# Kernel tuning notes

Measured on AMD Instinct MI355X. Metric: run time of the kernel, lower is better.

Reference implementation:

```python
import jax, jax.numpy as jnp
import numpy as np

B, S, D, P = 4, 2048, 1024, 1024

def setup_inputs() -> dict:
    key = jax.random.key(0)
    k1, k2, k3, k4 = jax.random.split(key, 4)
    x = jax.random.normal(k1, (B, S, D), dtype=jnp.float32)
    # nn.Linear weight is (out, in); store transposed (in, out) for x @ W
    scale = 1.0 / np.sqrt(D)
    Wq = jax.random.normal(k2, (D, P), dtype=jnp.float32) * scale
    Wk = jax.random.normal(k3, (D, P), dtype=jnp.float32) * scale
    Wv = jax.random.normal(k4, (D, P), dtype=jnp.float32) * scale
    return {"x": x, "Wq": Wq, "Wk": Wk, "Wv": Wv}

def reference(x, Wq, Wk, Wv):
    # projections (no bias)
    q = x @ Wq  # (B,S,P)
    k = x @ Wk
    v = x @ Wv
    scores = jnp.einsum('bsd,btd->bst', q, k)  # (B,S,S)
    seq = x.shape[1]
    causal = jnp.triu(jnp.ones((seq, seq), dtype=bool), k=1)
    scores = jnp.where(causal, -jnp.inf, scores)
    scores = scores / jnp.sqrt(jnp.asarray(P, dtype=scores.dtype))
    attn = jax.nn.softmax(scores, axis=-1)
    # dropout_prob=0.0 -> identity
    context = jnp.einsum('bst,btd->bsd', attn, v)  # (B,S,P)
    return context
```

## Files before the change

kernel.cpp:

```cpp
#include <hip/hip_runtime.h>
#include <hip/hip_bf16.h>


#define BDIM 4
#define SDIM 2048
#define DDIM 1024
#define PDIM 1024

typedef __attribute__((ext_vector_type(8))) short bf16x8;
typedef __attribute__((ext_vector_type(4))) float f32x4;

__device__ __forceinline__ unsigned short f2bf(float f) {
    union { float f; unsigned int u; } v; v.f = f;
    unsigned int u = v.u;
    unsigned int r = (u + 0x7fffu + ((u >> 16) & 1u)) >> 16;
    return (unsigned short)r;
}

__device__ __forceinline__ float bf2f(unsigned short h) {
    union { unsigned int u; float f; } v;
    v.u = ((unsigned int)h) << 16;
    return v.f;
}

__device__ __forceinline__ void async16(const unsigned short* g, unsigned short* l) {
    __builtin_amdgcn_global_load_lds(
        (const __attribute__((address_space(1))) unsigned int*)g,
        (__attribute__((address_space(3))) unsigned int*)l,
        16, 0, 0);
}

__device__ __forceinline__ void storeC(float* C, size_t idx, float v) { C[idx] = v; }
__device__ __forceinline__ void storeC(unsigned short* C, size_t idx, float v) { C[idx] = f2bf(v); }

__global__ __launch_bounds__(256) void prep_kernel(const float* __restrict__ x,
                                                   const float* __restrict__ W0,
                                                   const float* __restrict__ W1,
                                                   const float* __restrict__ W2,
                                                   unsigned short* __restrict__ Xb,
                                                   unsigned short* __restrict__ WT) {
    int bid = blockIdx.x;
    if (bid < 4096) {
        size_t i = (size_t)bid * 256 + threadIdx.x;
        float4 a = ((const float4*)x)[2 * i];
        float4 b = ((const float4*)x)[2 * i + 1];
        bf16x8 o;
        o[0] = (short)f2bf(a.x); o[1] = (short)f2bf(a.y);
        o[2] = (short)f2bf(a.z); o[3] = (short)f2bf(a.w);
        o[4] = (short)f2bf(b.x); o[5] = (short)f2bf(b.y);
        o[6] = (short)f2bf(b.z); o[7] = (short)f2bf(b.w);
        ((bf16x8*)Xb)[i] = o;
    } else {
        int idx = bid - 4096;
        int wz = idx >> 10;
        int t = idx & 1023;
        const float* W = (wz == 0) ? W0 : (wz == 1) ? W1 : W2;
        unsigned short* Tz = WT + (size_t)wz * DDIM * PDIM;
        __shared__ float tle[32][33];
        int c0 = (t & 31) * 32, r0 = (t >> 5) * 32;
        int tx = threadIdx.x & 31, ty = threadIdx.x >> 5;
        for (int i = ty; i < 32; i += 8)
            tle[i][tx] = W[(size_t)(r0 + i) * PDIM + c0 + tx];
        __syncthreads();
        for (int i = ty; i < 32; i += 8)
            Tz[(size_t)(c0 + i) * DDIM + r0 + tx] = f2bf(tle[tx][i]);
    }
}

__global__ __launch_bounds__(512, 2) void qkv256(
    const unsigned short* __restrict__ Xb,
    const unsigned short* __restrict__ WT,
    unsigned short* __restrict__ Q,
    unsigned short* __restrict__ Kb,
    unsigned short* __restrict__ VT) {
    const int BK = 64;
    const int TILE = 256 * BK;
    __shared__ __attribute__((aligned(16))) unsigned short smem[4 * TILE];

    int tm = blockIdx.y * 256;
    int tn = blockIdx.x * 256;

    int tid  = threadIdx.x;
    int lane = tid & 63;
    int wave = tid >> 6;
    int wr   = (wave >> 2) * 128;
    int wc   = (wave & 3) * 64;
    int quad = lane >> 4;
    int l16  = lane & 15;
    int rsw  = l16 & 7;

    f32x4 acc[8][4] = {};

    int srow = tid >> 3;
    int scol = ((tid & 7) ^ (srow & 7)) * 8;
    const unsigned short* Ag = Xb + (size_t)(tm + srow) * DDIM + scol;
    const unsigned short* Bg = WT + (size_t)(tn + srow) * DDIM + scol;

    auto issueTile = [&](int k0, int buf) {
        unsigned short* la = smem + buf * (2 * TILE) + tid * 8;
        unsigned short* lb = la + TILE;
#pragma unroll
        for (int p = 0; p < 4; p++) {
            async16(Ag + k0 + p * 64 * DDIM, la + p * 4096);
            async16(Bg + k0 + p * 64 * DDIM, lb + p * 4096);
        }
    };

    auto readA = [&](bf16x8 (&af)[4][2], const unsigned short* As, int mq) {
#pragma unroll
        for (int i2 = 0; i2 < 4; i2++)
#pragma unroll
            for (int s = 0; s < 2; s++)
                af[i2][s] = *(const bf16x8*)(As + (wr + mq * 64 + i2 * 16 + l16) * BK
                                                + ((s * 4 + quad) ^ rsw) * 8);
    };
    auto readB = [&](bf16x8 (&bfq)[2][2], const unsigned short* Bs, int nq) {
#pragma unroll
        for (int j2 = 0; j2 < 2; j2++)
#pragma unroll
            for (int s = 0; s < 2; s++)
                bfq[j2][s] = *(const bf16x8*)(Bs + (wc + nq * 32 + j2 * 16 + l16) * BK
                                                 + ((s * 4 + quad) ^ rsw) * 8);
    };
    auto mfmaQ = [&](const bf16x8 (&af)[4][2], const bf16x8 (&bfq)[2][2],
                     int mq, int nq) {
        __builtin_amdgcn_s_setprio(1);
#pragma unroll
        for (int s = 0; s < 2; s++)
#pragma unroll
            for (int i2 = 0; i2 < 4; i2++)
#pragma unroll
                for (int j2 = 0; j2 < 2; j2++)
                    acc[mq * 4 + i2][nq * 2 + j2] =
                        __builtin_amdgcn_mfma_f32_16x16x32_bf16(
                            af[i2][s], bfq[j2][s], acc[mq * 4 + i2][nq * 2 + j2],
                            0, 0, 0);
        __builtin_amdgcn_s_setprio(0);
    };

    const int nt = DDIM / BK;
    issueTile(0, 0);
    issueTile(BK, 1);
    asm volatile("s_waitcnt vmcnt(8)" ::: "memory");
    asm volatile("s_barrier" ::: "memory");

#pragma unroll 2
    for (int t = 0; t < nt; t++) {
        const unsigned short* As = smem + (t & 1) * (2 * TILE);
        const unsigned short* Bs = As + TILE;
        bf16x8 af[4][2];
        bf16x8 bfq[2][2];

        readA(af, As, 0);
        readB(bfq, Bs, 0);
        asm volatile("s_barrier" ::: "memory");
        mfmaQ(af, bfq, 0, 0);

        readB(bfq, Bs, 1);
        asm volatile("s_barrier" ::: "memory");
        mfmaQ(af, bfq, 0, 1);

        readA(af, As, 1);
        asm volatile("s_barrier" ::: "memory");
        mfmaQ(af, bfq, 1, 1);

        readB(bfq, Bs, 0);
        asm volatile("s_barrier" ::: "memory");
        mfmaQ(af, bfq, 1, 0);

        asm volatile("s_barrier" ::: "memory");
        if (t + 2 < nt) {
            issueTile((t + 2) * BK, t & 1);
            asm volatile("s_waitcnt vmcnt(8)" ::: "memory");
            asm volatile("s_barrier" ::: "memory");
        } else if (t + 1 < nt) {
            asm volatile("s_waitcnt vmcnt(0)" ::: "memory");
            asm volatile("s_barrier" ::: "memory");
        }
    }

    if (tn < 2048) {
        unsigned short* D = (tn < 1024) ? Q : Kb;
        int cbase = tn & 1023;
#pragma unroll
        for (int i = 0; i < 8; i++) {
            int r0 = tm + wr + (i >> 2) * 64 + (i & 3) * 16 + quad * 4;
#pragma unroll
            for (int j = 0; j < 4; j++) {
                int c = cbase + wc + (j >> 1) * 32 + (j & 1) * 16 + l16;
#pragma unroll
                for (int rr = 0; rr < 4; rr++)
                    D[(size_t)(r0 + rr) * 1024 + c] = f2bf(acc[i][j][rr]);
            }
        }
    } else {
        int b = tm >> 11;
        int s0 = tm & 2047;
        int vbase = tn - 2048;
        unsigned short* VTb = VT + (size_t)b * (PDIM * SDIM)
                                 + (size_t)vbase * SDIM + s0;
        const int TP = 264;
        unsigned short* T = smem;
#pragma unroll
        for (int sl = 0; sl < 8; sl++) {
            if ((wave & 3) == (sl >> 1)) {
                int jb = (sl & 1) * 2;
#pragma unroll
                for (int jj = 0; jj < 2; jj++) {
                    int j = jb + jj;
                    int cl = jj * 16 + l16;
#pragma unroll
                    for (int i = 0; i < 8; i++) {
                        int rl = wr + (i >> 2) * 64 + (i & 3) * 16 + quad * 4;
                        ushort4 w;
                        w.x = f2bf(acc[i][j][0]); w.y = f2bf(acc[i][j][1]);
                        w.z = f2bf(acc[i][j][2]); w.w = f2bf(acc[i][j][3]);
                        *(ushort4*)(T + cl * TP + rl) = w;
                    }
                }
            }
            __syncthreads();
            {
                int cl = tid >> 4;
                int sc = (tid & 15) * 16;
                bf16x8 u0 = *(const bf16x8*)(T + cl * TP + sc);
                bf16x8 u1 = *(const bf16x8*)(T + cl * TP + sc + 8);
                unsigned short* dst = VTb + (size_t)(sl * 32 + cl) * SDIM + sc;
                *(bf16x8*)dst = u0;
                *(bf16x8*)(dst + 8) = u1;
            }
            __syncthreads();
        }
    }
}

template <int LDA, int LDB, int LDC, int KMAX, int MODE, typename CT>
__global__ __launch_bounds__(256) void gemm_bt(
    const unsigned short* __restrict__ A0, const unsigned short* __restrict__ A1,
    long long sA,
    const unsigned short* __restrict__ B0, long long sB,
    CT* __restrict__ C0, CT* __restrict__ C1, long long sC,
    unsigned short* __restrict__ Kb, unsigned short* __restrict__ VT,
    float alpha) {
    const int BM = 128, BN = 128, BK = 64;
    const int ABUF = BM * BK;
    __shared__ __attribute__((aligned(16))) unsigned short smem[2 * ABUF + BN * BK];
    unsigned short* BsBuf = smem + 2 * ABUF;

    int tm, tn;
    if (MODE == 1) {
        int i = blockIdx.x;
        int t = (int)((sqrtf(8.f * i + 1.f) - 1.f) * 0.5f);
        if ((t + 1) * (t + 2) / 2 <= i) t++;
        if (t * (t + 1) / 2 > i) t--;
        tm = t * BM;
        tn = (i - t * (t + 1) / 2) * BN;
    } else if (MODE == 2) {
        int yy = (blockIdx.z < 2) ? ((int)gridDim.y - 1 - (int)blockIdx.y)
                                  : (int)blockIdx.y;
        tm = yy * BM;
        tn = blockIdx.x * BN;
    } else {
        tm = blockIdx.y * BM;
        tn = blockIdx.x * BN;
    }
    int kend = (MODE == 2) ? min(KMAX, tm + BM) : KMAX;

    int z = blockIdx.z;
    const unsigned short* A = (z < 2 ? A0 : A1) + (long long)(z & 1) * sA;
    const unsigned short* Bt = B0 + (long long)z * sB;
    CT* C = (z < 2 ? C0 : C1) + (long long)(z & 1) * sC;

    int tid  = threadIdx.x;
    int lane = tid & 63;
    int wave = tid >> 6;
    int wr   = (wave >> 1) * 64;
    int wc   = (wave & 1) * 64;
    int quad = lane >> 4;
    int l16  = lane & 15;
    int rsw  = l16 & 7;

    f32x4 acc[4][4] = {};

    int srow = tid >> 3;
    int scol = ((tid & 7) ^ (srow & 7)) * 8;
    const unsigned short* Ag = A + (size_t)(tm + srow) * LDA + scol;
    const unsigned short* Bg = Bt + (size_t)(tn + srow) * LDB + scol;

    auto issueA = [&](int k0, int buf) {
        unsigned short* la = smem + buf * ABUF + tid * 8;
        async16(Ag + k0, la);
        async16(Ag + k0 + 32 * LDA, la + 2048);
        async16(Ag + k0 + 64 * LDA, la + 4096);
        async16(Ag + k0 + 96 * LDA, la + 6144);
    };
    auto issueB = [&](int k0) {
        unsigned short* lb = BsBuf + tid * 8;
        async16(Bg + k0, lb);
        async16(Bg + k0 + 32 * LDB, lb + 2048);
        async16(Bg + k0 + 64 * LDB, lb + 4096);
        async16(Bg + k0 + 96 * LDB, lb + 6144);
    };

    auto kbody = [&](int i, int ns) {
        __syncthreads();
        bf16x8 bf[2][4];
#pragma unroll
        for (int s = 0; s < 2; s++)
#pragma unroll
            for (int j = 0; j < 4; j++)
                bf[s][j] = *(const bf16x8*)(BsBuf + (wc + j * 16 + l16) * BK
                                                  + ((s * 4 + quad) ^ rsw) * 8);
        __syncthreads();
        if (i + 1 < ns) { issueA((i + 1) * BK, (i + 1) & 1); issueB((i + 1) * BK); }
        const unsigned short* As = smem + (i & 1) * ABUF;
#pragma unroll
        for (int s = 0; s < 2; s++) {
            int chunk = ((s * 4 + quad) ^ rsw) * 8;
            bf16x8 af[4];
#pragma unroll
            for (int ii = 0; ii < 4; ii++)
                af[ii] = *(const bf16x8*)(As + (wr + ii * 16 + l16) * BK + chunk);
#pragma unroll
            for (int ii = 0; ii < 4; ii++)
#pragma unroll
                for (int j = 0; j < 4; j++)
                    acc[ii][j] = __builtin_amdgcn_mfma_f32_16x16x32_bf16(
                        af[ii], bf[s][j], acc[ii][j], 0, 0, 0);
        }
    };

    issueA(0, 0);
    issueB(0);
    if constexpr (MODE != 2) {
        constexpr int NS = KMAX / BK;
#pragma unroll
        for (int i = 0; i < NS; i++) kbody(i, NS);
    } else {
        int ns = kend / BK;
        for (int i = 0; i < ns; i++) kbody(i, ns);
    }

#pragma unroll
    for (int i = 0; i < 4; i++) {
        int r0 = tm + wr + i * 16 + quad * 4;
#pragma unroll
        for (int j = 0; j < 4; j++) {
            int c = tn + wc + j * 16 + l16;
#pragma unroll
            for (int rr = 0; rr < 4; rr++) {
                int r = r0 + rr;
                if (MODE == 1 && c > r) continue;
                storeC(C, (size_t)r * LDC + c, acc[i][j][rr] * alpha);
            }
        }
    }
}

__global__ __launch_bounds__(256) void softmax_causal(unsigned short* __restrict__ S01,
                                                      unsigned short* __restrict__ S23,
                                                      long long sS) {
    int row = blockIdx.x;
    int b = blockIdx.y;
    unsigned short* srow = (b < 2 ? S01 : S23) + (long long)(b & 1) * sS + (size_t)row * SDIM;
    int tid = threadIdx.x;
    int j0 = tid * 8;
    int valid = row + 1;
    int bound = ((row >> 7) + 1) << 7;
    bool active = j0 < valid;
    __shared__ float red[4];

    float f[8];
    if (active) {
        bf16x8 v8 = *(const bf16x8*)(srow + j0);
#pragma unroll
        for (int i = 0; i < 8; i++) f[i] = bf2f((unsigned short)v8[i]);
    }

    float m = -1e30f;
    if (active) {
#pragma unroll
        for (int i = 0; i < 8; i++) if (j0 + i < valid) m = fmaxf(m, f[i]);
    }
#pragma unroll
    for (int o = 32; o; o >>= 1) m = fmaxf(m, __shfl_xor(m, o, 64));
    if ((tid & 63) == 0) red[tid >> 6] = m;
    __syncthreads();
    m = fmaxf(fmaxf(red[0], red[1]), fmaxf(red[2], red[3]));
    __syncthreads();

    float e[8] = {0.f, 0.f, 0.f, 0.f, 0.f, 0.f, 0.f, 0.f};
    float l = 0.f;
    if (active) {
#pragma unroll
        for (int i = 0; i < 8; i++) {
            e[i] = (j0 + i < valid) ? __expf(f[i] - m) : 0.f;
            l += e[i];
        }
    }
#pragma unroll
    for (int o = 32; o; o >>= 1) l += __shfl_xor(l, o, 64);
    if ((tid & 63) == 0) red[tid >> 6] = l;
    __syncthreads();
    l = red[0] + red[1] + red[2] + red[3];
    float inv = 1.0f / l;

    if (j0 < bound) {
        bf16x8 o8;
#pragma unroll
        for (int i = 0; i < 8; i++) o8[i] = (short)f2bf(e[i] * inv);
        *(bf16x8*)(srow + j0) = o8;
    }
}

extern "C" void kernel_launch(void* const* d_in, const int* in_sizes, int n_in,
                              void* d_out, int out_size, void* d_ws, size_t ws_size,
                              hipStream_t stream) {
    const float* x  = (const float*)d_in[0];
    const float* Wq = (const float*)d_in[1];
    const float* Wk = (const float*)d_in[2];
    const float* Wv = (const float*)d_in[3];
    float* out = (float*)d_out;

    const size_t MS = (size_t)BDIM * SDIM;
    const long long SS = (long long)SDIM * SDIM;
    char* ws = (char*)d_ws;
    size_t off = 0;
    unsigned short* Xb   = (unsigned short*)(ws + off);
    unsigned short* S01  = Xb;                          off += MS * DDIM * 2;
    unsigned short* WT   = (unsigned short*)(ws + off); off += 3ull * DDIM * PDIM * 2;
    unsigned short* Q    = (unsigned short*)(ws + off); off += MS * PDIM * 2;
    unsigned short* Kb   = (unsigned short*)(ws + off); off += MS * PDIM * 2;
    unsigned short* VT   = (unsigned short*)(ws + off); off += MS * PDIM * 2;
    unsigned short* S23  = (unsigned short*)(ws + off); off += 2ull * SS * 2;

    prep_kernel<<<4096 + 3072, 256, 0, stream>>>(x, Wq, Wk, Wv, Xb, WT);

    qkv256<<<dim3(3 * PDIM / 256, MS / 256, 1), 512, 0, stream>>>(Xb, WT, Q, Kb, VT);

    const long long sQ = (long long)SDIM * PDIM;
    const float alpha = 1.0f / 32.0f;

    gemm_bt<PDIM, PDIM, SDIM, PDIM, 1, unsigned short>
        <<<dim3(136, 1, BDIM), 256, 0, stream>>>(
        Q, Q + 2 * sQ, sQ, Kb, sQ, S01, S23, SS, nullptr, nullptr, alpha);

    softmax_causal<<<dim3(SDIM, BDIM), 256, 0, stream>>>(S01, S23, SS);

    const long long sOut = (long long)SDIM * PDIM;
    gemm_bt<SDIM, SDIM, PDIM, SDIM, 2, float>
        <<<dim3(PDIM / 128, SDIM / 128, BDIM), 256, 0, stream>>>(
        S01, S23, SS, VT, sQ, out, out + 2 * sOut, sOut, nullptr, nullptr, 1.0f);
}
```

Measured before the change: 241.4 us.

## Split QKV GEMM tile loads into half-tile stages interleaved with MFMA quadrants

Rewrites the QKV projection GEMM main loop so each 128x64 half of the A and B tiles is staged separately. Prefetch of the next k-tile is issued between MFMA quadrants instead of in one burst at the end of the iteration. The warp-to-output mapping changes so each wave owns interleaved 64x32 sub-blocks, and explicit lgkmcnt waits plus sched_barriers pin the LDS-read/MFMA ordering. The aim is to hide global load latency and cut end-of-iteration stalls, at the cost of more barriers and a fragile hand-tuned vmcnt count. The diff also removes unused gemm_bt parameters and the dead MODE-0 branch.

```diff
diff --git a/kernel.cpp b/kernel.cpp
--- a/kernel.cpp
+++ b/kernel.cpp
@@ -67,15 +67,30 @@
     }
 }
 
-__global__ __launch_bounds__(512, 2) void qkv256(
+#define MMQ(MH, NH)                                                          \
+    do {                                                                     \
+        __builtin_amdgcn_s_setprio(1);                                       \
+        _Pragma("unroll") for (int ks = 0; ks < 2; ks++) {                   \
+            _Pragma("unroll") for (int mi = 0; mi < 4; mi++) {               \
+                _Pragma("unroll") for (int ni = 0; ni < 2; ni++) {           \
+                    acc[(MH) * 4 + mi][(NH) * 2 + ni] =                      \
+                        __builtin_amdgcn_mfma_f32_16x16x32_bf16(             \
+                            af[mi][ks], bf[ni][ks],                          \
+                            acc[(MH) * 4 + mi][(NH) * 2 + ni], 0, 0, 0);     \
+                }                                                            \
+            }                                                                \
+        }                                                                    \
+        __builtin_amdgcn_s_setprio(0);                                       \
+    } while (0)
+
+__global__ __launch_bounds__(512, 2) void qkv8p(
     const unsigned short* __restrict__ Xb,
     const unsigned short* __restrict__ WT,
     unsigned short* __restrict__ Q,
     unsigned short* __restrict__ Kb,
     unsigned short* __restrict__ VT) {
-    const int BK = 64;
-    const int TILE = 256 * BK;
-    __shared__ __attribute__((aligned(16))) unsigned short smem[4 * TILE];
+    const int HALF = 128 * 64;
+    __shared__ __attribute__((aligned(16))) unsigned short smem[8 * HALF];
 
     int tm = blockIdx.y * 256;
     int tn = blockIdx.x * 256;
@@ -83,8 +98,8 @@
     int tid  = threadIdx.x;
     int lane = tid & 63;
     int wave = tid >> 6;
-    int wr   = (wave >> 2) * 128;
-    int wc   = (wave & 3) * 64;
+    int wm   = wave >> 2;
+    int wn   = wave & 3;
     int quad = lane >> 4;
     int l16  = lane & 15;
     int rsw  = l16 & 7;
@@ -96,87 +111,85 @@
     const unsigned short* Ag = Xb + (size_t)(tm + srow) * DDIM + scol;
     const unsigned short* Bg = WT + (size_t)(tn + srow) * DDIM + scol;
 
-    auto issueTile = [&](int k0, int buf) {
-        unsigned short* la = smem + buf * (2 * TILE) + tid * 8;
-        unsigned short* lb = la + TILE;
-#pragma unroll
-        for (int p = 0; p < 4; p++) {
-            async16(Ag + k0 + p * 64 * DDIM, la + p * 4096);
-            async16(Bg + k0 + p * 64 * DDIM, lb + p * 4096);
-        }
-    };
-
-    auto readA = [&](bf16x8 (&af)[4][2], const unsigned short* As, int mq) {
-#pragma unroll
-        for (int i2 = 0; i2 < 4; i2++)
-#pragma unroll
-            for (int s = 0; s < 2; s++)
-                af[i2][s] = *(const bf16x8*)(As + (wr + mq * 64 + i2 * 16 + l16) * BK
-                                                + ((s * 4 + quad) ^ rsw) * 8);
-    };
-    auto readB = [&](bf16x8 (&bfq)[2][2], const unsigned short* Bs, int nq) {
-#pragma unroll
-        for (int j2 = 0; j2 < 2; j2++)
-#pragma unroll
-            for (int s = 0; s < 2; s++)
-                bfq[j2][s] = *(const bf16x8*)(Bs + (wc + nq * 32 + j2 * 16 + l16) * BK
-                                                 + ((s * 4 + quad) ^ rsw) * 8);
-    };
-    auto mfmaQ = [&](const bf16x8 (&af)[4][2], const bf16x8 (&bfq)[2][2],
-                     int mq, int nq) {
-        __builtin_amdgcn_s_setprio(1);
-#pragma unroll
-        for (int s = 0; s < 2; s++)
-#pragma unroll
-            for (int i2 = 0; i2 < 4; i2++)
-#pragma unroll
-                for (int j2 = 0; j2 < 2; j2++)
-                    acc[mq * 4 + i2][nq * 2 + j2] =
-                        __builtin_amdgcn_mfma_f32_16x16x32_bf16(
-                            af[i2][s], bfq[j2][s], acc[mq * 4 + i2][nq * 2 + j2],
-                            0, 0, 0);
-        __builtin_amdgcn_s_setprio(0);
-    };
-
-    const int nt = DDIM / BK;
-    issueTile(0, 0);
-    issueTile(BK, 1);
-    asm volatile("s_waitcnt vmcnt(8)" ::: "memory");
-    asm volatile("s_barrier" ::: "memory");
+    auto slotPtr = [&](int buf, int isB, int h) {
+        return smem + (size_t)(((buf * 2 + isB) * 2 + h)) * HALF;
+    };
+    auto stage = [&](int buf, int isB, int h, int kt) {
+        const unsigned short* g = (isB ? Bg : Ag) + (size_t)(h * 128) * DDIM + kt * 64;
+        unsigned short* l = slotPtr(buf, isB, h) + tid * 8;
+        async16(g, l);
+        async16(g + 64 * DDIM, l + 4096);
+    };
+    auto dsA = [&](bf16x8 (&af)[4][2], int buf, int h) {
+        const unsigned short* p = slotPtr(buf, 0, h);
+#pragma unroll
+        for (int mi = 0; mi < 4; mi++)
+#pragma unroll
+            for (int ks = 0; ks < 2; ks++)
+                af[mi][ks] = *(const bf16x8*)(p + (wm * 64 + mi * 16 + l16) * 64
+                                                + ((ks * 4 + quad) ^ rsw) * 8);
+    };
+    auto dsB = [&](bf16x8 (&bf)[2][2], int buf, int h) {
+        const unsigned short* p = slotPtr(buf, 1, h);
+#pragma unroll
+        for (int ni = 0; ni < 2; ni++)
+#pragma unroll
+            for (int ks = 0; ks < 2; ks++)
+                bf[ni][ks] = *(const bf16x8*)(p + (wn * 32 + ni * 16 + l16) * 64
+                                                + ((ks * 4 + quad) ^ rsw) * 8);
+    };
+
+    const int nt = DDIM / 64;
+    stage(0, 0, 0, 0); stage(0, 1, 0, 0); stage(0, 1, 1, 0); stage(0, 0, 1, 0);
+    asm volatile("s_waitcnt vmcnt(4)" ::: "memory");
+    stage(1, 0, 0, 1); stage(1, 1, 1, 1); stage(1, 0, 1, 1);
+    asm volatile("s_waitcnt vmcnt(6)" ::: "memory");
+    __builtin_amdgcn_s_barrier();
 
 #pragma unroll 2
     for (int t = 0; t < nt; t++) {
-        const unsigned short* As = smem + (t & 1) * (2 * TILE);
-        const unsigned short* Bs = As + TILE;
+        int b = t & 1, o = b ^ 1;
         bf16x8 af[4][2];
-        bf16x8 bfq[2][2];
-
-        readA(af, As, 0);
-        readB(bfq, Bs, 0);
-        asm volatile("s_barrier" ::: "memory");
-        mfmaQ(af, bfq, 0, 0);
-
-        readB(bfq, Bs, 1);
-        asm volatile("s_barrier" ::: "memory");
-        mfmaQ(af, bfq, 0, 1);
-
-        readA(af, As, 1);
-        asm volatile("s_barrier" ::: "memory");
-        mfmaQ(af, bfq, 1, 1);
-
-        readB(bfq, Bs, 0);
-        asm volatile("s_barrier" ::: "memory");
-        mfmaQ(af, bfq, 1, 0);
-
-        asm volatile("s_barrier" ::: "memory");
+        bf16x8 bf[2][2];
+
+        dsA(af, b, 0);
+        dsB(bf, b, 0);
+        if (t + 1 < nt) stage(o, 1, 0, t + 1);
+        asm volatile("s_waitcnt lgkmcnt(8)" ::: "memory");
+        __builtin_amdgcn_s_barrier();
+        asm volatile("s_waitcnt lgkmcnt(0)" ::: "memory");
+        __builtin_amdgcn_sched_barrier(0);
+        MMQ(0, 0);
+        __builtin_amdgcn_s_barrier();
+
+        dsB(bf, b, 1);
+        if (t + 2 < nt) stage(b, 0, 0, t + 2);
+        __builtin_amdgcn_s_barrier();
+        asm volatile("s_waitcnt lgkmcnt(0)" ::: "memory");
+        __builtin_amdgcn_sched_barrier(0);
+        MMQ(0, 1);
+        __builtin_amdgcn_s_barrier();
+
+        dsA(af, b, 1);
+        if (t + 2 < nt) stage(b, 1, 1, t + 2);
+        __builtin_amdgcn_s_barrier();
+        asm volatile("s_waitcnt lgkmcnt(0)" ::: "memory");
+        __builtin_amdgcn_sched_barrier(0);
+        MMQ(1, 1);
+        __builtin_amdgcn_s_barrier();
+
+        dsB(bf, b, 0);
+        if (t + 2 < nt) stage(b, 0, 1, t + 2);
+        __builtin_amdgcn_s_barrier();
+        asm volatile("s_waitcnt lgkmcnt(0)" ::: "memory");
+        __builtin_amdgcn_sched_barrier(0);
+        MMQ(1, 0);
         if (t + 2 < nt) {
-            issueTile((t + 2) * BK, t & 1);
-            asm volatile("s_waitcnt vmcnt(8)" ::: "memory");
-            asm volatile("s_barrier" ::: "memory");
+            asm volatile("s_waitcnt vmcnt(6)" ::: "memory");
         } else if (t + 1 < nt) {
             asm volatile("s_waitcnt vmcnt(0)" ::: "memory");
-            asm volatile("s_barrier" ::: "memory");
-        }
+        }
+        __builtin_amdgcn_s_barrier();
     }
 
     if (tn < 2048) {
@@ -184,34 +197,34 @@
         int cbase = tn & 1023;
 #pragma unroll
         for (int i = 0; i < 8; i++) {
-            int r0 = tm + wr + (i >> 2) * 64 + (i & 3) * 16 + quad * 4;
+            int r0 = tm + (i >> 2) * 128 + wm * 64 + (i & 3) * 16 + quad * 4;
 #pragma unroll
             for (int j = 0; j < 4; j++) {
-                int c = cbase + wc + (j >> 1) * 32 + (j & 1) * 16 + l16;
+                int c = cbase + (j >> 1) * 128 + wn * 32 + (j & 1) * 16 + l16;
 #pragma unroll
                 for (int rr = 0; rr < 4; rr++)
                     D[(size_t)(r0 + rr) * 1024 + c] = f2bf(acc[i][j][rr]);
             }
         }
     } else {
-        int b = tm >> 11;
+        int bb = tm >> 11;
         int s0 = tm & 2047;
         int vbase = tn - 2048;
-        unsigned short* VTb = VT + (size_t)b * (PDIM * SDIM)
+        unsigned short* VTb = VT + (size_t)bb * (PDIM * SDIM)
                                  + (size_t)vbase * SDIM + s0;
         const int TP = 264;
         unsigned short* T = smem;
 #pragma unroll
         for (int sl = 0; sl < 8; sl++) {
-            if ((wave & 3) == (sl >> 1)) {
-                int jb = (sl & 1) * 2;
-#pragma unroll
-                for (int jj = 0; jj < 2; jj++) {
-                    int j = jb + jj;
-                    int cl = jj * 16 + l16;
+            if (wn == (sl & 3)) {
+                int nh = sl >> 2;
+#pragma unroll
+                for (int ni = 0; ni < 2; ni++) {
+                    int j = nh * 2 + ni;
+                    int cl = ni * 16 + l16;
 #pragma unroll
                     for (int i = 0; i < 8; i++) {
-                        int rl = wr + (i >> 2) * 64 + (i & 3) * 16 + quad * 4;
+                        int rl = (i >> 2) * 128 + wm * 64 + (i & 3) * 16 + quad * 4;
                         ushort4 w;
                         w.x = f2bf(acc[i][j][0]); w.y = f2bf(acc[i][j][1]);
                         w.z = f2bf(acc[i][j][2]); w.w = f2bf(acc[i][j][3]);
@@ -240,7 +253,6 @@
     long long sA,
     const unsigned short* __restrict__ B0, long long sB,
     CT* __restrict__ C0, CT* __restrict__ C1, long long sC,
-    unsigned short* __restrict__ Kb, unsigned short* __restrict__ VT,
     float alpha) {
     const int BM = 128, BN = 128, BK = 64;
     const int ABUF = BM * BK;
@@ -255,13 +267,10 @@
         if (t * (t + 1) / 2 > i) t--;
         tm = t * BM;
         tn = (i - t * (t + 1) / 2) * BN;
-    } else if (MODE == 2) {
+    } else {
         int yy = (blockIdx.z < 2) ? ((int)gridDim.y - 1 - (int)blockIdx.y)
                                   : (int)blockIdx.y;
         tm = yy * BM;
-        tn = blockIdx.x * BN;
-    } else {
-        tm = blockIdx.y * BM;
         tn = blockIdx.x * BN;
     }
     int kend = (MODE == 2) ? min(KMAX, tm + BM) : KMAX;
@@ -436,19 +445,19 @@
 
     prep_kernel<<<4096 + 3072, 256, 0, stream>>>(x, Wq, Wk, Wv, Xb, WT);
 
-    qkv256<<<dim3(3 * PDIM / 256, MS / 256, 1), 512, 0, stream>>>(Xb, WT, Q, Kb, VT);
+    qkv8p<<<dim3(3 * PDIM / 256, MS / 256, 1), 512, 0, stream>>>(Xb, WT, Q, Kb, VT);
 
     const long long sQ = (long long)SDIM * PDIM;
     const float alpha = 1.0f / 32.0f;
 
     gemm_bt<PDIM, PDIM, SDIM, PDIM, 1, unsigned short>
         <<<dim3(136, 1, BDIM), 256, 0, stream>>>(
-        Q, Q + 2 * sQ, sQ, Kb, sQ, S01, S23, SS, nullptr, nullptr, alpha);
+        Q, Q + 2 * sQ, sQ, Kb, sQ, S01, S23, SS, alpha);
 
     softmax_causal<<<dim3(SDIM, BDIM), 256, 0, stream>>>(S01, S23, SS);
 
     const long long sOut = (long long)SDIM * PDIM;
     gemm_bt<SDIM, SDIM, PDIM, SDIM, 2, float>
         <<<dim3(PDIM / 128, SDIM / 128, BDIM), 256, 0, stream>>>(
-        S01, S23, SS, VT, sQ, out, out + 2 * sOut, sOut, nullptr, nullptr, 1.0f);
-}
+        S01, S23, SS, VT, sQ, out, out + 2 * sOut, sOut, 1.0f);
+}
```

New measurement: 238.1 us. Within noise of the previous version (-1.3%).
